# Performance work log

Measured on AMD Instinct MI355X. Metric: run time of the kernel, lower is better.

Reference implementation:

```python
import jax, jax.numpy as jnp
import numpy as np

N = 100000   # nodes
E = 1600000  # edges
D = 128      # input_dim
H = 128      # hidden_dim
O = 128      # output_dim
G = 64       # graphs in batch
BN_EPS = 1e-5


def setup_inputs() -> dict:
    key = jax.random.key(0)
    ks = jax.random.split(key, 32)
    x = jax.random.normal(ks[0], (N, D), jnp.float32)
    edge_index = jax.random.randint(ks[1], (2, E), 0, N, dtype=jnp.int64)
    batch = jnp.sort(jax.random.randint(ks[2], (N,), 0, G, dtype=jnp.int64))

    def lin_w(k, fan_in, fan_out):
        return (jax.random.normal(k, (fan_in, fan_out), jnp.float32) / np.sqrt(fan_in)).astype(jnp.float32)

    def lin_b(k, fan_out):
        return (0.01 * jax.random.normal(k, (fan_out,), jnp.float32)).astype(jnp.float32)

    def bn(k, dim):
        k1, k2, k3, k4 = jax.random.split(k, 4)
        gamma = 1.0 + 0.1 * jax.random.normal(k1, (dim,), jnp.float32)
        beta = 0.1 * jax.random.normal(k2, (dim,), jnp.float32)
        mean = 0.1 * jax.random.normal(k3, (dim,), jnp.float32)
        var = 0.5 + jax.random.uniform(k4, (dim,), jnp.float32)
        return gamma, beta, mean, var

    inp = {
        "x": x, "edge_index": edge_index, "batch": batch,
        "w11": lin_w(ks[3], D, H), "b11": lin_b(ks[4], H),
        "w12": lin_w(ks[5], H, H), "b12": lin_b(ks[6], H),
        "w21": lin_w(ks[7], H, H), "b21": lin_b(ks[8], H),
        "w22": lin_w(ks[9], H, H), "b22": lin_b(ks[10], H),
        "w31": lin_w(ks[11], H, H), "b31": lin_b(ks[12], H),
        "w32": lin_w(ks[13], H, O), "b32": lin_b(ks[14], O),
    }
    g1, be1, m1, v1 = bn(ks[15], H)
    g2, be2, m2, v2 = bn(ks[16], H)
    g3, be3, m3, v3 = bn(ks[17], O)
    inp.update({"bn1_g": g1, "bn1_b": be1, "bn1_m": m1, "bn1_v": v1,
                "bn2_g": g2, "bn2_b": be2, "bn2_m": m2, "bn2_v": v2,
                "bn3_g": g3, "bn3_b": be3, "bn3_m": m3, "bn3_v": v3})
    return inp


def _gin_conv(x, src, dst, wa, ba, wb, bb):
    # sum-aggregate neighbor features: out[i] = x[i] + sum_{(j->i) in E} x[j]  (eps=0)
    agg = jax.ops.segment_sum(x[src], dst, num_segments=N)
    h = x + agg
    # 2-layer MLP: Linear -> ReLU -> Linear
    return jax.nn.relu(h @ wa + ba) @ wb + bb


def _bn_eval(x, g, b, m, v):
    return (x - m) * (g * jax.lax.rsqrt(v + BN_EPS)) + b


def reference(x, edge_index, batch,
              w11, b11, w12, b12, w21, b21, w22, b22, w31, b31, w32, b32,
              bn1_g, bn1_b, bn1_m, bn1_v,
              bn2_g, bn2_b, bn2_m, bn2_v,
              bn3_g, bn3_b, bn3_m, bn3_v):
    src, dst = edge_index[0], edge_index[1]
    h = _gin_conv(x, src, dst, w11, b11, w12, b12)
    h = jax.nn.relu(_bn_eval(h, bn1_g, bn1_b, bn1_m, bn1_v))  # dropout: eval-mode identity
    h = _gin_conv(h, src, dst, w21, b21, w22, b22)
    h = jax.nn.relu(_bn_eval(h, bn2_g, bn2_b, bn2_m, bn2_v))
    h = _gin_conv(h, src, dst, w31, b31, w32, b32)
    h = jax.nn.relu(_bn_eval(h, bn3_g, bn3_b, bn3_m, bn3_v))
    # global mean pool over each graph
    sums = jax.ops.segment_sum(h, batch, num_segments=G)
    counts = jax.ops.segment_sum(jnp.ones((N,), h.dtype), batch, num_segments=G)
    return sums / jnp.maximum(counts, 1.0)[:, None]
```

## Files before the change

### kernel.cpp

```cpp
#include <hip/hip_runtime.h>
#include <hip/hip_bf16.h>
#include <cstdint>

static constexpr int D = 128;
static constexpr int SPANB = 9;
static constexpr int CHUNK = 4096;

typedef __bf16 v8bf __attribute__((ext_vector_type(8)));
typedef float  v4f  __attribute__((ext_vector_type(4)));

__device__ inline float bflo(unsigned u) { return __uint_as_float(u << 16); }
__device__ inline float bfhi(unsigned u) { return __uint_as_float(u & 0xffff0000u); }
__device__ inline unsigned short bfbits(float f) {
    __hip_bfloat16 h = __float2bfloat16(f);
    return *reinterpret_cast<unsigned short*>(&h);
}
__device__ inline unsigned packbf(float a, float b) {
    return (unsigned)bfbits(a) | ((unsigned)bfbits(b) << 16);
}

__global__ __launch_bounds__(256) void prep_kernel(
    const float* __restrict__ w11, const float* __restrict__ w12,
    const float* __restrict__ w21, const float* __restrict__ w22,
    const float* __restrict__ w31, const float* __restrict__ w32,
    __hip_bfloat16* __restrict__ Wp,
    const float* bn1g, const float* bn1b, const float* bn1m, const float* bn1v, const float* lb1,
    const float* bn2g, const float* bn2b, const float* bn2m, const float* bn2v, const float* lb2,
    const float* bn3g, const float* bn3b, const float* bn3m, const float* bn3v, const float* lb3,
    float* sc1, float* sh1, float* sc2, float* sh2, float* sc3, float* sh3,
    const float* __restrict__ x, __hip_bfloat16* __restrict__ xb, long long n8,
    const int* __restrict__ dst, int* __restrict__ blockhist, int nE, int nblk) {
    int b = blockIdx.x, t = threadIdx.x;
    if (b < 48) {
        int idx = b * 256 + t;
        int widx = idx >> 11, r = idx & 2047;
        const float* W = widx == 0 ? w11 : widx == 1 ? w12 : widx == 2 ? w21
                       : widx == 3 ? w22 : widx == 4 ? w31 : w32;
        int l = r & 63, cf = (r >> 6) & 7, ks = r >> 9;
        int k0 = ks * 32 + (l >> 4) * 8, c = cf * 16 + (l & 15);
        unsigned o0 = packbf(W[(k0 + 0) * D + c], W[(k0 + 1) * D + c]);
        unsigned o1 = packbf(W[(k0 + 2) * D + c], W[(k0 + 3) * D + c]);
        unsigned o2 = packbf(W[(k0 + 4) * D + c], W[(k0 + 5) * D + c]);
        unsigned o3 = packbf(W[(k0 + 6) * D + c], W[(k0 + 7) * D + c]);
        reinterpret_cast<uint4*>(Wp + (size_t)idx * 8)[0] = make_uint4(o0, o1, o2, o3);
    } else if (b < 51) {
        if (t < D) {
            int j = b - 48;
            const float *g, *bb, *m, *v, *lb;
            float *sc, *sh;
            if (j == 0)      { g = bn1g; bb = bn1b; m = bn1m; v = bn1v; lb = lb1; sc = sc1; sh = sh1; }
            else if (j == 1) { g = bn2g; bb = bn2b; m = bn2m; v = bn2v; lb = lb2; sc = sc2; sh = sh2; }
            else             { g = bn3g; bb = bn3b; m = bn3m; v = bn3v; lb = lb3; sc = sc3; sh = sh3; }
            float s = g[t] * rsqrtf(v[t] + 1e-5f);
            sc[t] = s;
            sh[t] = (lb[t] - m[t]) * s + bb[t];
        }
    } else if (b < 51 + nblk) {
        __shared__ int h[256];
        h[t] = 0;
        __syncthreads();
        int base = (b - 51) * CHUNK;
#pragma unroll
        for (int i = 0; i < CHUNK / 256; ++i) {
            int e = base + i * 256 + t;
            if (e < nE) atomicAdd(&h[dst[e] >> SPANB], 1);
        }
        __syncthreads();
        blockhist[(b - 51) * 256 + t] = h[t];
    } else {
        long long i = (long long)(b - 51 - nblk) * 256 + t;
        if (i < n8) {
            const float4* f4 = reinterpret_cast<const float4*>(x);
            float4 a = f4[i * 2], bb = f4[i * 2 + 1];
            uint4 o = make_uint4(packbf(a.x, a.y), packbf(a.z, a.w),
                                 packbf(bb.x, bb.y), packbf(bb.z, bb.w));
            reinterpret_cast<uint4*>(xb)[i] = o;
        }
    }
}

__global__ __launch_bounds__(256) void bscan_kernel(int* __restrict__ blockhist,
                                                    int* __restrict__ totals, int nblk) {
    __shared__ int s[256];
    int b = blockIdx.x, t = threadIdx.x;
    int running = 0;
    for (int base = 0; base < nblk; base += 256) {
        int idx = base + t;
        int v = (idx < nblk) ? blockhist[idx * 256 + b] : 0;
        s[t] = v;
        __syncthreads();
#pragma unroll
        for (int off = 1; off < 256; off <<= 1) {
            int add = (t >= off) ? s[t - off] : 0;
            __syncthreads();
            s[t] += add;
            __syncthreads();
        }
        if (idx < nblk) blockhist[idx * 256 + b] = running + s[t] - v;
        int tot = s[255];
        __syncthreads();
        running += tot;
    }
    if (t == 0) totals[b] = running;
}

__global__ void tscan_kernel(const int* __restrict__ totals,
                             int* __restrict__ bucketbase, int nbuk, int nE) {
    __shared__ int s[256];
    int t = threadIdx.x;
    int v = (t < nbuk) ? totals[t] : 0;
    s[t] = v;
    __syncthreads();
#pragma unroll
    for (int off = 1; off < 256; off <<= 1) {
        int add = (t >= off) ? s[t - off] : 0;
        __syncthreads();
        s[t] += add;
        __syncthreads();
    }
    if (t < nbuk) bucketbase[t] = s[t] - v;
    if (t == 0) bucketbase[nbuk] = nE;
}

__global__ __launch_bounds__(256) void fill2_kernel(const int* __restrict__ src,
                                                    const int* __restrict__ dst,
                                                    const int* __restrict__ blockhist,
                                                    const int* __restrict__ bucketbase,
                                                    unsigned* __restrict__ records,
                                                    int nE, int nbuk) {
    __shared__ int cur[256];
    int t = threadIdx.x;
    if (t < nbuk) cur[t] = bucketbase[t] + blockhist[blockIdx.x * 256 + t];
    __syncthreads();
    int base = blockIdx.x * CHUNK;
#pragma unroll
    for (int i = 0; i < CHUNK / 256; ++i) {
        int e = base + i * 256 + t;
        if (e < nE) {
            int d = dst[e], s = src[e];
            int p = atomicAdd(&cur[d >> SPANB], 1);
            records[p] = ((unsigned)s << SPANB) | (unsigned)(d & ((1 << SPANB) - 1));
        }
    }
}

__global__ __launch_bounds__(512) void csr2_kernel(const unsigned* __restrict__ records,
                                                   const int* __restrict__ bucketbase,
                                                   int* __restrict__ rowptr,
                                                   int* __restrict__ col,
                                                   int nN, int nE) {
    __shared__ int cnt[512];
    __shared__ int cur[512];
    int b = blockIdx.x, t = threadIdx.x;
    int node0 = b << SPANB;
    cnt[t] = 0;
    __syncthreads();
    int rbeg = bucketbase[b], rend = bucketbase[b + 1];
    for (int r = rbeg + t; r < rend; r += 512)
        atomicAdd(&cnt[records[r] & ((1 << SPANB) - 1)], 1);
    __syncthreads();
    int v = cnt[t];
#pragma unroll
    for (int off = 1; off < 512; off <<= 1) {
        int add = (t >= off) ? cnt[t - off] : 0;
        __syncthreads();
        cnt[t] += add;
        __syncthreads();
    }
    int pos = rbeg + cnt[t] - v;
    if (node0 + t < nN) rowptr[node0 + t] = pos;
    if (b == 0 && t == 0) rowptr[nN] = nE;
    cur[t] = pos;
    __syncthreads();
    for (int r = rbeg + t; r < rend; r += 512) {
        unsigned rec = records[r];
        int p = atomicAdd(&cur[rec & ((1 << SPANB) - 1)], 1);
        col[p] = (int)(rec >> SPANB);
    }
}

#define ACC8(vv) { a[0]+=bflo(vv.x); a[1]+=bfhi(vv.x); a[2]+=bflo(vv.y); a[3]+=bfhi(vv.y); \
                   a[4]+=bflo(vv.z); a[5]+=bfhi(vv.z); a[6]+=bflo(vv.w); a[7]+=bfhi(vv.w); }

__global__ __launch_bounds__(256) void agg_kernel(const __hip_bfloat16* __restrict__ h,
                                                  __hip_bfloat16* __restrict__ S,
                                                  const int* __restrict__ rowptr,
                                                  const int* __restrict__ col, int nN) {
    int node = blockIdx.x * 16 + (threadIdx.x >> 4);
    if (node >= nN) return;
    int q = threadIdx.x & 15;
    const uint4* h4 = reinterpret_cast<const uint4*>(h);
    uint4 u = h4[(size_t)node * 16 + q];
    float a[8];
    a[0] = bflo(u.x); a[1] = bfhi(u.x); a[2] = bflo(u.y); a[3] = bfhi(u.y);
    a[4] = bflo(u.z); a[5] = bfhi(u.z); a[6] = bflo(u.w); a[7] = bfhi(u.w);
    int beg = rowptr[node], end = rowptr[node + 1];
    int j = beg;
    for (; j + 3 < end; j += 4) {
        int s0 = col[j], s1 = col[j + 1], s2 = col[j + 2], s3 = col[j + 3];
        uint4 v0 = h4[(size_t)s0 * 16 + q];
        uint4 v1 = h4[(size_t)s1 * 16 + q];
        uint4 v2 = h4[(size_t)s2 * 16 + q];
        uint4 v3 = h4[(size_t)s3 * 16 + q];
        ACC8(v0); ACC8(v1); ACC8(v2); ACC8(v3);
    }
    for (; j < end; ++j) {
        uint4 v0 = h4[(size_t)col[j] * 16 + q];
        ACC8(v0);
    }
    uint4 o = make_uint4(packbf(a[0], a[1]), packbf(a[2], a[3]),
                         packbf(a[4], a[5]), packbf(a[6], a[7]));
    reinterpret_cast<uint4*>(S)[(size_t)node * 16 + q] = o;
}

__global__ __launch_bounds__(256) void mlp3_kernel(
    const __hip_bfloat16* __restrict__ S,
    const __hip_bfloat16* __restrict__ WpA,
    const __hip_bfloat16* __restrict__ WpB,
    const float* __restrict__ b1,
    const float* __restrict__ sc, const float* __restrict__ sh,
    __hip_bfloat16* __restrict__ out, int nN) {
    __shared__ __attribute__((aligned(16))) char Wl[32768];
    __shared__ __attribute__((aligned(16))) char Ml[4][4096];
    int t = threadIdx.x;
    int w = t >> 6, l = t & 63;
    int q2 = l >> 4, r16 = l & 15;
    int row0 = blockIdx.x * 64 + w * 16;
    int row = row0 + r16;
    int ar = row < nN ? row : nN - 1;

    v8bf bfrag[4];
#pragma unroll
    for (int ks = 0; ks < 4; ++ks)
        bfrag[ks] = *reinterpret_cast<const v8bf*>(S + (size_t)ar * D + ks * 32 + q2 * 8);

    uint4* wl = reinterpret_cast<uint4*>(Wl);
    const uint4* wa4 = reinterpret_cast<const uint4*>(WpA);
    const uint4* wb4 = reinterpret_cast<const uint4*>(WpB);

#pragma unroll
    for (int i = 0; i < 8; ++i) wl[i * 256 + t] = wa4[i * 256 + t];
    __syncthreads();

    const v8bf* wv = reinterpret_cast<const v8bf*>(Wl);
    const float4* b14 = reinterpret_cast<const float4*>(b1);
    const float4* sc4 = reinterpret_cast<const float4*>(sc);
    const float4* sh4 = reinterpret_cast<const float4*>(sh);
    char* mid = Ml[w];
    int swz = (r16 & 7) << 4;

    v4f acc[8] = {};
#pragma unroll
    for (int ks = 0; ks < 4; ++ks) {
#pragma unroll
        for (int cf = 0; cf < 8; ++cf)
            acc[cf] = __builtin_amdgcn_mfma_f32_16x16x32_bf16(
                wv[(ks * 8 + cf) * 64 + l], bfrag[ks], acc[cf], 0, 0, 0);
    }
#pragma unroll
    for (int cf = 0; cf < 8; ++cf) {
        float4 bb = b14[cf * 4 + q2];
        float e0 = fmaxf(acc[cf][0] + bb.x, 0.f);
        float e1 = fmaxf(acc[cf][1] + bb.y, 0.f);
        float e2 = fmaxf(acc[cf][2] + bb.z, 0.f);
        float e3 = fmaxf(acc[cf][3] + bb.w, 0.f);
        int waddr = r16 * 256 + ((cf * 32 + q2 * 8) ^ swz);
        *reinterpret_cast<uint2*>(mid + waddr) = make_uint2(packbf(e0, e1), packbf(e2, e3));
    }
    __syncthreads();

#pragma unroll
    for (int i = 0; i < 8; ++i) wl[i * 256 + t] = wb4[i * 256 + t];
    __syncthreads();

    v4f acc2[8] = {};
#pragma unroll
    for (int ks = 0; ks < 4; ++ks) {
        v8bf mfrag = *reinterpret_cast<v8bf*>(mid + r16 * 256 + ((ks * 64 + q2 * 16) ^ swz));
#pragma unroll
        for (int cf = 0; cf < 8; ++cf)
            acc2[cf] = __builtin_amdgcn_mfma_f32_16x16x32_bf16(
                wv[(ks * 8 + cf) * 64 + l], mfrag, acc2[cf], 0, 0, 0);
    }
#pragma unroll
    for (int cf = 0; cf < 8; ++cf) {
        float4 s0 = sc4[cf * 4 + q2], s1 = sh4[cf * 4 + q2];
        float e0 = fmaxf(acc2[cf][0] * s0.x + s1.x, 0.f);
        float e1 = fmaxf(acc2[cf][1] * s0.y + s1.y, 0.f);
        float e2 = fmaxf(acc2[cf][2] * s0.z + s1.z, 0.f);
        float e3 = fmaxf(acc2[cf][3] * s0.w + s1.w, 0.f);
        int waddr = r16 * 256 + ((cf * 32 + q2 * 8) ^ swz);
        *reinterpret_cast<uint2*>(mid + waddr) = make_uint2(packbf(e0, e1), packbf(e2, e3));
    }
    {
        int q = l & 15;
#pragma unroll
        for (int i = 0; i < 4; ++i) {
            int r = (l >> 4) * 4 + i;
            int grow = row0 + r;
            if (grow < nN) {
                uint4 v = *reinterpret_cast<uint4*>(mid + r * 256 + ((q * 16) ^ ((r & 7) << 4)));
                reinterpret_cast<uint4*>(out + (size_t)grow * D)[q] = v;
            }
        }
    }
}

__global__ __launch_bounds__(1024) void pool2_kernel(const __hip_bfloat16* __restrict__ h,
                                                     const int* __restrict__ batch,
                                                     float* __restrict__ out, int nN) {
    int g = blockIdx.x;
    int lo, hi;
    {
        int a = 0, b = nN;
        while (a < b) { int mid = (a + b) >> 1; if (batch[mid] < g) a = mid + 1; else b = mid; }
        lo = a;
        b = nN;
        while (a < b) { int mid = (a + b) >> 1; if (batch[mid] < g + 1) a = mid + 1; else b = mid; }
        hi = a;
    }
    int grp = threadIdx.x >> 4;
    int q = threadIdx.x & 15;
    float a[8] = {};
    const uint4* h4 = reinterpret_cast<const uint4*>(h);
    for (int i = lo + grp; i < hi; i += 64) {
        uint4 v = h4[(size_t)i * 16 + q];
        ACC8(v);
    }
    __shared__ float red[64][130];
#pragma unroll
    for (int k = 0; k < 8; ++k) red[grp][q * 8 + k] = a[k];
    __syncthreads();
    int t = threadIdx.x;
    if (t < D) {
        float s = 0.f;
#pragma unroll 8
        for (int r = 0; r < 64; ++r) s += red[r][t];
        out[(size_t)g * D + t] = s / fmaxf((float)(hi - lo), 1.f);
    }
}

extern "C" void kernel_launch(void* const* d_in, const int* in_sizes, int n_in,
                              void* d_out, int out_size, void* d_ws, size_t ws_size,
                              hipStream_t stream) {
    const float* x    = (const float*)d_in[0];
    const int*   ei   = (const int*)d_in[1];
    const int*   batch= (const int*)d_in[2];
    const float* w11 = (const float*)d_in[3];  const float* b11 = (const float*)d_in[4];
    const float* w12 = (const float*)d_in[5];  const float* b12 = (const float*)d_in[6];
    const float* w21 = (const float*)d_in[7];  const float* b21 = (const float*)d_in[8];
    const float* w22 = (const float*)d_in[9];  const float* b22 = (const float*)d_in[10];
    const float* w31 = (const float*)d_in[11]; const float* b31 = (const float*)d_in[12];
    const float* w32 = (const float*)d_in[13]; const float* b32 = (const float*)d_in[14];
    const float* bn1g = (const float*)d_in[15]; const float* bn1b = (const float*)d_in[16];
    const float* bn1m = (const float*)d_in[17]; const float* bn1v = (const float*)d_in[18];
    const float* bn2g = (const float*)d_in[19]; const float* bn2b = (const float*)d_in[20];
    const float* bn2m = (const float*)d_in[21]; const float* bn2v = (const float*)d_in[22];
    const float* bn3g = (const float*)d_in[23]; const float* bn3b = (const float*)d_in[24];
    const float* bn3m = (const float*)d_in[25]; const float* bn3v = (const float*)d_in[26];

    int nN = in_sizes[0] / D;
    int nE = in_sizes[1] / 2;
    int nG = out_size / D;

    const int* srcp = ei;
    const int* dstp = ei + nE;

    size_t NB2 = (size_t)nN * D * sizeof(__hip_bfloat16);
    char* ws = (char*)d_ws;
    __hip_bfloat16* A16 = (__hip_bfloat16*)ws;
    __hip_bfloat16* B16 = (__hip_bfloat16*)(ws + NB2);
    __hip_bfloat16* S16 = (__hip_bfloat16*)(ws + 2 * NB2);
    __hip_bfloat16* Wp  = (__hip_bfloat16*)(ws + 3 * NB2);
    size_t wp_bytes = 6 * 2048 * 8 * sizeof(__hip_bfloat16);
    char* auxp = ws + 3 * NB2 + wp_bytes;
    size_t aux_bytes = 16384;
    float* sc1 = (float*)auxp + 0,   *sh1 = (float*)auxp + 128;
    float* sc2 = (float*)auxp + 256, *sh2 = (float*)auxp + 384;
    float* sc3 = (float*)auxp + 512, *sh3 = (float*)auxp + 640;
    int*   bucketbase = (int*)(auxp + (768 + 64) * 4);
    int*   totals     = bucketbase + 300;
    int* rowptr = (int*)(auxp + aux_bytes);
    int* col    = rowptr + (nN + 1);

    unsigned* records = (unsigned*)S16;
    int* blockhist    = (int*)((char*)S16 + (size_t)nE * 4);

    int nbuk = (nN + 511) >> SPANB;
    int nblk = (nE + CHUNK - 1) / CHUNK;
    long long n8 = (long long)nN * D / 8;
    int cvtBlocks = (int)((n8 + 255) / 256);

    prep_kernel<<<51 + nblk + cvtBlocks, 256, 0, stream>>>(
        w11, w12, w21, w22, w31, w32, Wp,
        bn1g, bn1b, bn1m, bn1v, b12,
        bn2g, bn2b, bn2m, bn2v, b22,
        bn3g, bn3b, bn3m, bn3v, b32,
        sc1, sh1, sc2, sh2, sc3, sh3,
        x, A16, n8,
        dstp, blockhist, nE, nblk);

    bscan_kernel<<<nbuk, 256, 0, stream>>>(blockhist, totals, nblk);
    tscan_kernel<<<1, 256, 0, stream>>>(totals, bucketbase, nbuk, nE);
    fill2_kernel<<<nblk, 256, 0, stream>>>(srcp, dstp, blockhist, bucketbase, records, nE, nbuk);
    csr2_kernel<<<nbuk, 512, 0, stream>>>(records, bucketbase, rowptr, col, nN, nE);

    int aggBlocks = (nN + 15) / 16;
    int mlpBlocks = (nN + 63) / 64;
    __hip_bfloat16* Wp1 = Wp + 0 * 16384; __hip_bfloat16* Wp2 = Wp + 1 * 16384;
    __hip_bfloat16* Wp3 = Wp + 2 * 16384; __hip_bfloat16* Wp4 = Wp + 3 * 16384;
    __hip_bfloat16* Wp5 = Wp + 4 * 16384; __hip_bfloat16* Wp6 = Wp + 5 * 16384;

    agg_kernel<<<aggBlocks, 256, 0, stream>>>(A16, S16, rowptr, col, nN);
    mlp3_kernel<<<mlpBlocks, 256, 0, stream>>>(S16, Wp1, Wp2, b11, sc1, sh1, B16, nN);

    agg_kernel<<<aggBlocks, 256, 0, stream>>>(B16, S16, rowptr, col, nN);
    mlp3_kernel<<<mlpBlocks, 256, 0, stream>>>(S16, Wp3, Wp4, b21, sc2, sh2, A16, nN);

    agg_kernel<<<aggBlocks, 256, 0, stream>>>(A16, S16, rowptr, col, nN);
    mlp3_kernel<<<mlpBlocks, 256, 0, stream>>>(S16, Wp5, Wp6, b31, sc3, sh3, B16, nN);

    pool2_kernel<<<nG, 1024, 0, stream>>>(B16, batch, (float*)d_out, nN);
}
```

Before: 303.5 us.

## Split aggregation feature dimension into halves across interleaved blocks

The neighbor aggregation kernel now gives each node 8 threads covering half of the 128 features, so each block handles 32 nodes for one feature half. Block indices are interleaved so that the two halves of the same node tile run in consecutive blocks, which should keep each gathered row in L2 until its second half is read. Each gather becomes a 128-byte segment instead of 256 bytes, and the number of independent row loads in flight per thread grows. In exchange, every node's rowptr and col entries are read twice, and each gather request brings in less data.

```diff
diff --git a/kernel.cpp b/kernel.cpp
--- a/kernel.cpp
+++ b/kernel.cpp
@@ -182,15 +182,20 @@
 #define ACC8(vv) { a[0]+=bflo(vv.x); a[1]+=bfhi(vv.x); a[2]+=bflo(vv.y); a[3]+=bfhi(vv.y); \
                    a[4]+=bflo(vv.z); a[5]+=bfhi(vv.z); a[6]+=bflo(vv.w); a[7]+=bfhi(vv.w); }
 
-__global__ __launch_bounds__(256) void agg_kernel(const __hip_bfloat16* __restrict__ h,
-                                                  __hip_bfloat16* __restrict__ S,
-                                                  const int* __restrict__ rowptr,
-                                                  const int* __restrict__ col, int nN) {
-    int node = blockIdx.x * 16 + (threadIdx.x >> 4);
+__global__ __launch_bounds__(256) void aggh_kernel(const __hip_bfloat16* __restrict__ h,
+                                                   __hip_bfloat16* __restrict__ S,
+                                                   const int* __restrict__ rowptr,
+                                                   const int* __restrict__ col,
+                                                   int nN, int nT) {
+    int b8 = blockIdx.x & 7;
+    int half = b8 >> 2;
+    int tile = (blockIdx.x >> 3) * 4 + (b8 & 3);
+    if (tile >= nT) return;
+    int node = tile * 32 + (threadIdx.x >> 3);
     if (node >= nN) return;
-    int q = threadIdx.x & 15;
+    int off = half * 8 + (threadIdx.x & 7);
     const uint4* h4 = reinterpret_cast<const uint4*>(h);
-    uint4 u = h4[(size_t)node * 16 + q];
+    uint4 u = h4[(size_t)node * 16 + off];
     float a[8];
     a[0] = bflo(u.x); a[1] = bfhi(u.x); a[2] = bflo(u.y); a[3] = bfhi(u.y);
     a[4] = bflo(u.z); a[5] = bfhi(u.z); a[6] = bflo(u.w); a[7] = bfhi(u.w);
@@ -198,19 +203,19 @@
     int j = beg;
     for (; j + 3 < end; j += 4) {
         int s0 = col[j], s1 = col[j + 1], s2 = col[j + 2], s3 = col[j + 3];
-        uint4 v0 = h4[(size_t)s0 * 16 + q];
-        uint4 v1 = h4[(size_t)s1 * 16 + q];
-        uint4 v2 = h4[(size_t)s2 * 16 + q];
-        uint4 v3 = h4[(size_t)s3 * 16 + q];
+        uint4 v0 = h4[(size_t)s0 * 16 + off];
+        uint4 v1 = h4[(size_t)s1 * 16 + off];
+        uint4 v2 = h4[(size_t)s2 * 16 + off];
+        uint4 v3 = h4[(size_t)s3 * 16 + off];
         ACC8(v0); ACC8(v1); ACC8(v2); ACC8(v3);
     }
     for (; j < end; ++j) {
-        uint4 v0 = h4[(size_t)col[j] * 16 + q];
+        uint4 v0 = h4[(size_t)col[j] * 16 + off];
         ACC8(v0);
     }
     uint4 o = make_uint4(packbf(a[0], a[1]), packbf(a[2], a[3]),
                          packbf(a[4], a[5]), packbf(a[6], a[7]));
-    reinterpret_cast<uint4*>(S)[(size_t)node * 16 + q] = o;
+    reinterpret_cast<uint4*>(S)[(size_t)node * 16 + off] = o;
 }
 
 __global__ __launch_bounds__(256) void mlp3_kernel(
@@ -405,19 +410,20 @@
     fill2_kernel<<<nblk, 256, 0, stream>>>(srcp, dstp, blockhist, bucketbase, records, nE, nbuk);
     csr2_kernel<<<nbuk, 512, 0, stream>>>(records, bucketbase, rowptr, col, nN, nE);
 
-    int aggBlocks = (nN + 15) / 16;
+    int nT = (nN + 31) / 32;
+    int aggBlocks = ((nT + 3) / 4) * 8;
     int mlpBlocks = (nN + 63) / 64;
     __hip_bfloat16* Wp1 = Wp + 0 * 16384; __hip_bfloat16* Wp2 = Wp + 1 * 16384;
     __hip_bfloat16* Wp3 = Wp + 2 * 16384; __hip_bfloat16* Wp4 = Wp + 3 * 16384;
     __hip_bfloat16* Wp5 = Wp + 4 * 16384; __hip_bfloat16* Wp6 = Wp + 5 * 16384;
 
-    agg_kernel<<<aggBlocks, 256, 0, stream>>>(A16, S16, rowptr, col, nN);
+    aggh_kernel<<<aggBlocks, 256, 0, stream>>>(A16, S16, rowptr, col, nN, nT);
     mlp3_kernel<<<mlpBlocks, 256, 0, stream>>>(S16, Wp1, Wp2, b11, sc1, sh1, B16, nN);
 
-    agg_kernel<<<aggBlocks, 256, 0, stream>>>(B16, S16, rowptr, col, nN);
+    aggh_kernel<<<aggBlocks, 256, 0, stream>>>(B16, S16, rowptr, col, nN, nT);
     mlp3_kernel<<<mlpBlocks, 256, 0, stream>>>(S16, Wp3, Wp4, b21, sc2, sh2, A16, nN);
 
-    agg_kernel<<<aggBlocks, 256, 0, stream>>>(A16, S16, rowptr, col, nN);
+    aggh_kernel<<<aggBlocks, 256, 0, stream>>>(A16, S16, rowptr, col, nN, nT);
     mlp3_kernel<<<mlpBlocks, 256, 0, stream>>>(S16, Wp5, Wp6, b31, sc3, sh3, B16, nN);
 
     pool2_kernel<<<nG, 1024, 0, stream>>>(B16, batch, (float*)d_out, nN);
```

After: 289.6 us, median of 2. 1.05x faster.
